# Optimization experiments

Hardware: AMD Instinct MI355X
Metric: run time of the kernel (lower is better)

## Reference

```python
import jax, jax.numpy as jnp
import numpy as np

N_FREQS = 6  # PositionEmbedding default used by LISA


def setup_inputs() -> dict:
    key = jax.random.key(0)
    ks = jax.random.split(key, 8)
    B, L, N, D, H = 8, 32768, 2048, 64, 256
    in_dim = 1 * (2 * N_FREQS + 1) + 3 * D  # 13 + 192 = 205

    def w(k, i, o):
        return jax.random.normal(k, (i, o), jnp.float32) * (1.0 / np.sqrt(i))

    return {
        "coord": jax.random.uniform(ks[0], (B, L, 1), jnp.float32),
        "latent": jax.random.normal(ks[1], (B, N, D), jnp.float32),
        "W0": w(ks[2], in_dim, H), "b0": jnp.zeros((H,), jnp.float32),
        "W1": w(ks[3], H, H), "b1": jnp.zeros((H,), jnp.float32),
        "W2": w(ks[4], H, H), "b2": jnp.zeros((H,), jnp.float32),
        "W3": w(ks[5], H, H), "b3": jnp.zeros((H,), jnp.float32),
        "W4": w(ks[6], H, 1), "b4": jnp.zeros((1,), jnp.float32),
    }


def reference(coord, latent, W0, b0, W1, b1, W2, b2, W3, b3, W4, b4):
    B, N, D = latent.shape
    # feat_unfold: concat shifted-prev / self / shifted-next along channels
    feat = jnp.swapaxes(latent, 1, 2)                                   # [B, D, N]
    feat_prev = jnp.concatenate([feat[:, :, :1], feat[:, :, :-1]], axis=2)
    feat_next = jnp.concatenate([feat[:, :, 1:], feat[:, :, -1:]], axis=2)
    feat = jnp.concatenate([feat_prev, feat, feat_next], axis=1)        # [B, 3D, N]

    # grid_sample(bilinear, padding_mode='border', align_corners=False) on a
    # 1-row image: y coordinate 0 hits row 0 exactly, so only x interpolates.
    # torch mapping: ix = ((gx + 1) * W - 1) / 2 with gx = coord*2 - 1
    ix = coord[..., 0] * N - 0.5                                        # [B, L]
    x0 = jnp.floor(ix)
    t = ix - x0                                                         # lerp weight
    i0 = jnp.clip(x0.astype(jnp.int32), 0, N - 1)                       # border clamp
    i1 = jnp.clip(x0.astype(jnp.int32) + 1, 0, N - 1)
    f0 = jnp.take_along_axis(feat, i0[:, None, :], axis=2)              # [B, 3D, L]
    f1 = jnp.take_along_axis(feat, i1[:, None, :], axis=2)
    sampled = (1.0 - t)[:, None, :] * f0 + t[:, None, :] * f1
    sampled = jnp.swapaxes(sampled, 1, 2)                               # [B, L, 3D]

    # positional encoding: [x, sin(f x), cos(f x) for f in 1,2,4,8,16,32]
    freqs = 2.0 ** jnp.arange(N_FREQS, dtype=jnp.float32)
    ang = coord * freqs                                                 # [B, L, 6]
    pe = jnp.stack([jnp.sin(ang), jnp.cos(ang)], axis=-1)
    pe = pe.reshape(ang.shape[0], ang.shape[1], 2 * N_FREQS)            # [B, L, 12]

    inp = jnp.concatenate([coord, pe, sampled], axis=-1)                # [B, L, 205]

    h = jax.nn.relu(inp @ W0 + b0)
    h = jax.nn.relu(h @ W1 + b1)
    h = jax.nn.relu(h @ W2 + b2)
    h = jax.nn.relu(h @ W3 + b3)
    return h @ W4 + b4                                                  # [B, L, 1]
```

## Files before the change

kernel.cpp:

```cpp
#include <hip/hip_runtime.h>

typedef unsigned short ushort_t;
typedef unsigned int uint_t;
typedef __attribute__((ext_vector_type(8))) short short8;
typedef __attribute__((ext_vector_type(4))) float float4v;
typedef __attribute__((ext_vector_type(4))) uint_t uint4v;

#define NLAT 2048
#define DLAT 64

#define PW_BASE 128
#define PW0_OFF 0
#define PW1_OFF 57344
#define PW2_OFF 122880
#define PW3_OFF 188416
#define H7 28672
#define H8 32768

__device__ __forceinline__ float b2f(ushort_t u) {
  union { uint_t i; float f; } v; v.i = ((uint_t)u) << 16; return v.f;
}
__device__ __forceinline__ ushort_t f2b(float f) {
  uint_t x = __float_as_uint(f);
  uint_t r = (x + 0x7fffu + ((x >> 16) & 1u)) >> 16;
  return (ushort_t)r;
}
__device__ __forceinline__ uint_t pack2(float lo, float hi) {
  return (uint_t)f2b(lo) | ((uint_t)f2b(hi) << 16);
}
__device__ __forceinline__ int imin(int a, int b) { return a < b ? a : b; }
__device__ __forceinline__ int imax(int a, int b) { return a > b ? a : b; }

__device__ __forceinline__ float ldv(const float* p, long i)    { return p[i]; }
__device__ __forceinline__ float ldv(const ushort_t* p, long i) { return b2f(p[i]); }
__device__ __forceinline__ void stv(float* p, long i, float v)    { p[i] = v; }
__device__ __forceinline__ void stv(ushort_t* p, long i, float v) { p[i] = f2b(v); }

__device__ __forceinline__ float4 load4f(const float* p) { return *(const float4*)p; }
__device__ __forceinline__ float4 load4f(const ushort_t* p) {
  uint2 u = *(const uint2*)p;
  float4 r;
  r.x = b2f((ushort_t)(u.x & 0xffffu)); r.y = b2f((ushort_t)(u.x >> 16));
  r.z = b2f((ushort_t)(u.y & 0xffffu)); r.w = b2f((ushort_t)(u.y >> 16));
  return r;
}

__device__ __forceinline__ void async_copy16(const ushort_t* g, ushort_t* l) {
  __builtin_amdgcn_global_load_lds(
      (const __attribute__((address_space(1))) void*)g,
      (__attribute__((address_space(3))) void*)l, 16, 0, 0);
}
__device__ __forceinline__ void stage_half(ushort_t* dst, const ushort_t* src,
                                           int chunks, int tid) {
  for (int k = 0; k < chunks; ++k) {
    int i = tid + (k << 9);
    async_copy16(src + (size_t)i * 8, dst + (size_t)i * 8);
  }
}

__global__ void detect_mode(const ushort_t* __restrict__ lat, int* __restrict__ flag) {
  if (threadIdx.x == 0) *flag = 0;
  __syncthreads();
  int big = 0;
  for (int i = threadIdx.x; i < 1024; i += 64) {
    float v = b2f(lat[i]);
    if (!(fabsf(v) < 1e5f)) big = 1;
  }
  if (__any(big) && threadIdx.x == 0) *flag = 1;
}

template <typename TI>
__global__ void pack_w_t(const TI* __restrict__ W0, const TI* __restrict__ W1,
                         const TI* __restrict__ W2, const TI* __restrict__ W3,
                         ushort_t* __restrict__ pw, const int* __restrict__ flag, int want)
{
  if (*flag != want) return;
  int g = blockIdx.x * blockDim.x + threadIdx.x;
  if (g >= 31 * 1024) return;
  int lane = g & 63, q = lane >> 4;
  int mt   = (g >> 6) & 15;
  int ktg  = g >> 10;
  const TI* W; ushort_t* dst; int kt, KT; bool isw0 = false;
  if (ktg < 7)       { W = W0; dst = pw + PW0_OFF; kt = ktg;      KT = 7; isw0 = true; }
  else if (ktg < 15) { W = W1; dst = pw + PW1_OFF; kt = ktg - 7;  KT = 8; }
  else if (ktg < 23) { W = W2; dst = pw + PW2_OFF; kt = ktg - 15; KT = 8; }
  else               { W = W3; dst = pw + PW3_OFF; kt = ktg - 23; KT = 8; }
  int col = mt * 16 + (lane & 15);
  uint_t words[4];
#pragma unroll
  for (int h = 0; h < 4; ++h) {
    ushort_t vv[2];
#pragma unroll
    for (int e = 0; e < 2; ++e) {
      int j = 2 * h + e;
      int f = 32 * kt + 16 * (j >> 2) + 4 * q + (j & 3);
      int row = f;
      if (isw0) row = (f < 192) ? (13 + f) : (f == 192 ? 0 : (f <= 204 ? f - 192 : -1));
      vv[e] = (row >= 0) ? f2b(ldv(W, (long)row * 256 + col)) : (ushort_t)0;
    }
    words[h] = (uint_t)vv[0] | ((uint_t)vv[1] << 16);
  }
  uint4 o; o.x = words[0]; o.y = words[1]; o.z = words[2]; o.w = words[3];
  *(uint4*)(dst + ((size_t)(mt * KT + kt) * 64 + lane) * 8) = o;
}

template <int KT, int MTBASE>
__device__ __forceinline__ void compute_half(float4v (&acc)[16][2],
                                             const uint4v (&hu)[8][2],
                                             const ushort_t* buf, int lane)
{
#pragma unroll
  for (int m = 0; m < 8; ++m) {
    acc[MTBASE + m][0] = (float4v){0.f, 0.f, 0.f, 0.f};
    acc[MTBASE + m][1] = (float4v){0.f, 0.f, 0.f, 0.f};
  }
#pragma unroll
  for (int kt = 0; kt < KT; ++kt) {
    short8 b0 = __builtin_bit_cast(short8, hu[kt][0]);
    short8 b1 = __builtin_bit_cast(short8, hu[kt][1]);
#pragma unroll
    for (int m = 0; m < 8; ++m) {
      short8 a = *(const short8*)&buf[((size_t)(m * KT + kt) * 64 + lane) * 8];
      acc[MTBASE + m][0] = __builtin_amdgcn_mfma_f32_16x16x32_bf16(a, b0, acc[MTBASE + m][0], 0, 0, 0);
      acc[MTBASE + m][1] = __builtin_amdgcn_mfma_f32_16x16x32_bf16(a, b1, acc[MTBASE + m][1], 0, 0, 0);
    }
  }
}

__device__ __forceinline__ void convert_layer(float4v (&acc)[16][2], uint4v (&hu)[8][2],
                                              const float* bwl, int q)
{
#pragma unroll
  for (int mt = 0; mt < 16; ++mt) {
    float4 b4 = *(const float4*)&bwl[mt * 16 + 4 * q];
#pragma unroll
    for (int g = 0; g < 2; ++g) {
      float v0 = fmaxf(acc[mt][g][0] + b4.x, 0.f);
      float v1 = fmaxf(acc[mt][g][1] + b4.y, 0.f);
      float v2 = fmaxf(acc[mt][g][2] + b4.z, 0.f);
      float v3 = fmaxf(acc[mt][g][3] + b4.w, 0.f);
      hu[mt >> 1][g][(mt & 1) * 2 + 0] = pack2(v0, v1);
      hu[mt >> 1][g][(mt & 1) * 2 + 1] = pack2(v2, v3);
    }
  }
}

template <typename TI>
__global__ __launch_bounds__(512, 2) void lisa_fused_t(
    const TI* __restrict__ coord, const TI* __restrict__ latent,
    const TI* __restrict__ bias0, const TI* __restrict__ bias1,
    const TI* __restrict__ bias2, const TI* __restrict__ bias3,
    const TI* __restrict__ W4,    const TI* __restrict__ b4,
    const ushort_t* __restrict__ pw, TI* __restrict__ out,
    const int* __restrict__ flag, int want)
{
  if (*flag != want) return;
  __shared__ __align__(16) ushort_t wbuf[2][H8];
  __shared__ __align__(16) float bw[4 * 256 + 256 + 1];

  const int tid  = threadIdx.x;
  const int lane = tid & 63, q = lane >> 4, m15 = lane & 15;
  const int wv   = tid >> 6;
  const long pbase = (long)blockIdx.x * 256 + wv * 32 + m15;

  stage_half(wbuf[0], pw + PW0_OFF, 7, tid);
  for (int i = tid; i < 1281; i += 512) {
    float v;
    if (i < 256)       v = ldv(bias0, i);
    else if (i < 512)  v = ldv(bias1, i - 256);
    else if (i < 768)  v = ldv(bias2, i - 512);
    else if (i < 1024) v = ldv(bias3, i - 768);
    else if (i < 1280) v = ldv(W4, i - 1024);
    else               v = ldv(b4, 0);
    bw[i] = v;
  }

  uint4v hu[8][2];
#pragma unroll
  for (int g = 0; g < 2; ++g) {
    long p = pbase + g * 16;
    float c   = ldv(coord, p);
    float ixv = c * 2048.0f - 0.5f;
    float x0f = floorf(ixv);
    float t   = ixv - x0f;
    int   x0  = (int)x0f;
    int   i0  = imin(imax(x0, 0), NLAT - 1);
    int   i1  = imin(imax(x0 + 1, 0), NLAT - 1);
    float w0 = 1.0f - t, w1 = t;
    int rows0[3] = { imax(i0 - 1, 0), i0, imin(i0 + 1, NLAT - 1) };
    int rows1[3] = { imax(i1 - 1, 0), i1, imin(i1 + 1, NLAT - 1) };
    const TI* lat = latent + (size_t)(p >> 15) * (NLAT * DLAT);
#pragma unroll
    for (int tb = 0; tb < 12; ++tb) {
      int region = tb >> 2;
      int d0 = 16 * (tb & 3) + 4 * q;
      float4 a = load4f(lat + (long)rows0[region] * DLAT + d0);
      float4 b = load4f(lat + (long)rows1[region] * DLAT + d0);
      hu[tb >> 1][g][(tb & 1) * 2 + 0] = pack2(w0 * a.x + w1 * b.x, w0 * a.y + w1 * b.y);
      hu[tb >> 1][g][(tb & 1) * 2 + 1] = pack2(w0 * a.z + w1 * b.z, w0 * a.w + w1 * b.w);
    }
    float pv[4];
#pragma unroll
    for (int s = 0; s < 4; ++s) {
      int f = 192 + 4 * q + s;
      float v = 0.0f;
      if (f == 192) v = c;
      else if (f <= 204) {
        int i = f - 193;
        float fr = (float)(1 << (i >> 1));
        float ang = c * fr;
        v = (i & 1) ? __cosf(ang) : __sinf(ang);
      }
      pv[s] = v;
    }
    hu[6][g][0] = pack2(pv[0], pv[1]);
    hu[6][g][1] = pack2(pv[2], pv[3]);
    hu[6][g][2] = 0; hu[6][g][3] = 0;
  }
  __syncthreads();

  float4v acc[16][2];

  stage_half(wbuf[1], pw + PW0_OFF + H7, 7, tid);
  compute_half<7, 0>(acc, hu, wbuf[0], lane);
  __syncthreads();
  stage_half(wbuf[0], pw + PW1_OFF, 8, tid);
  compute_half<7, 8>(acc, hu, wbuf[1], lane);
  convert_layer(acc, hu, bw + 0 * 256, q);
  __syncthreads();

  stage_half(wbuf[1], pw + PW1_OFF + H8, 8, tid);
  compute_half<8, 0>(acc, hu, wbuf[0], lane);
  __syncthreads();
  stage_half(wbuf[0], pw + PW2_OFF, 8, tid);
  compute_half<8, 8>(acc, hu, wbuf[1], lane);
  convert_layer(acc, hu, bw + 1 * 256, q);
  __syncthreads();

  stage_half(wbuf[1], pw + PW2_OFF + H8, 8, tid);
  compute_half<8, 0>(acc, hu, wbuf[0], lane);
  __syncthreads();
  stage_half(wbuf[0], pw + PW3_OFF, 8, tid);
  compute_half<8, 8>(acc, hu, wbuf[1], lane);
  convert_layer(acc, hu, bw + 2 * 256, q);
  __syncthreads();

  stage_half(wbuf[1], pw + PW3_OFF + H8, 8, tid);
  compute_half<8, 0>(acc, hu, wbuf[0], lane);
  __syncthreads();
  compute_half<8, 8>(acc, hu, wbuf[1], lane);

  float partial0 = 0.f, partial1 = 0.f;
#pragma unroll
  for (int mt = 0; mt < 16; ++mt) {
    float4 b3v = *(const float4*)&bw[3 * 256 + mt * 16 + 4 * q];
    float4 w4v = *(const float4*)&bw[1024 + mt * 16 + 4 * q];
    float v;
    v = fmaxf(acc[mt][0][0] + b3v.x, 0.f); partial0 += v * w4v.x;
    v = fmaxf(acc[mt][0][1] + b3v.y, 0.f); partial0 += v * w4v.y;
    v = fmaxf(acc[mt][0][2] + b3v.z, 0.f); partial0 += v * w4v.z;
    v = fmaxf(acc[mt][0][3] + b3v.w, 0.f); partial0 += v * w4v.w;
    v = fmaxf(acc[mt][1][0] + b3v.x, 0.f); partial1 += v * w4v.x;
    v = fmaxf(acc[mt][1][1] + b3v.y, 0.f); partial1 += v * w4v.y;
    v = fmaxf(acc[mt][1][2] + b3v.z, 0.f); partial1 += v * w4v.z;
    v = fmaxf(acc[mt][1][3] + b3v.w, 0.f); partial1 += v * w4v.w;
  }
  partial0 += __shfl_xor(partial0, 16, 64);
  partial0 += __shfl_xor(partial0, 32, 64);
  partial1 += __shfl_xor(partial1, 16, 64);
  partial1 += __shfl_xor(partial1, 32, 64);
  if (lane < 16) {
    float bb = bw[1280];
    stv(out, pbase,      partial0 + bb);
    stv(out, pbase + 16, partial1 + bb);
  }
}

extern "C" void kernel_launch(void* const* d_in, const int* in_sizes, int n_in,
                              void* d_out, int out_size, void* d_ws, size_t ws_size,
                              hipStream_t stream) {
  int* flag = (int*)d_ws;
  ushort_t* pw = (ushort_t*)d_ws + PW_BASE;

  detect_mode<<<1, 64, 0, stream>>>((const ushort_t*)d_in[1], flag);

  pack_w_t<float><<<62, 512, 0, stream>>>(
      (const float*)d_in[2], (const float*)d_in[4], (const float*)d_in[6],
      (const float*)d_in[8], pw, flag, 1);
  lisa_fused_t<float><<<1024, 512, 0, stream>>>(
      (const float*)d_in[0], (const float*)d_in[1],
      (const float*)d_in[3], (const float*)d_in[5], (const float*)d_in[7],
      (const float*)d_in[9], (const float*)d_in[10], (const float*)d_in[11],
      pw, (float*)d_out, flag, 1);

  pack_w_t<ushort_t><<<62, 512, 0, stream>>>(
      (const ushort_t*)d_in[2], (const ushort_t*)d_in[4], (const ushort_t*)d_in[6],
      (const ushort_t*)d_in[8], pw, flag, 0);
  lisa_fused_t<ushort_t><<<1024, 512, 0, stream>>>(
      (const ushort_t*)d_in[0], (const ushort_t*)d_in[1],
      (const ushort_t*)d_in[3], (const ushort_t*)d_in[5], (const ushort_t*)d_in[7],
      (const ushort_t*)d_in[9], (const ushort_t*)d_in[10], (const ushort_t*)d_in[11],
      pw, (ushort_t*)d_out, flag, 0);
}
```

Measured before the change: 258.6 us.

## Stream weights in 32-column chunks with ping-pong activations and smaller blocks

Each layer is now processed in 8 output chunks of 32 features. A small double-buffered LDS tile (2x16KB) is refilled per chunk, and activations ping-pong between two register arrays instead of a 16x2 accumulator array. Blocks shrink from 512 to 256 threads with launch bounds of 3 blocks/CU and twice as many blocks, aiming for lower LDS and register use and higher occupancy. In exchange there are many more __syncthreads barriers (one per chunk), and each barrier has less MFMA work to hide weight-load latency.

```diff
diff --git a/kernel.cpp b/kernel.cpp
--- a/kernel.cpp
+++ b/kernel.cpp
@@ -14,8 +14,6 @@
 #define PW1_OFF 57344
 #define PW2_OFF 122880
 #define PW3_OFF 188416
-#define H7 28672
-#define H8 32768
 
 __device__ __forceinline__ float b2f(ushort_t u) {
   union { uint_t i; float f; } v; v.i = ((uint_t)u) << 16; return v.f;
@@ -50,11 +48,19 @@
       (const __attribute__((address_space(1))) void*)g,
       (__attribute__((address_space(3))) void*)l, 16, 0, 0);
 }
-__device__ __forceinline__ void stage_half(ushort_t* dst, const ushort_t* src,
-                                           int chunks, int tid) {
-  for (int k = 0; k < chunks; ++k) {
-    int i = tid + (k << 9);
-    async_copy16(src + (size_t)i * 8, dst + (size_t)i * 8);
+
+__device__ __forceinline__ void stage_idx(int gi, ushort_t* dst,
+                                          const ushort_t* __restrict__ pw, int tid) {
+  int layer = gi >> 3, c = gi & 7;
+  int KT = (gi < 8) ? 7 : 8;
+  int loff = (layer == 0) ? PW0_OFF : (layer == 1) ? PW1_OFF
+           : (layer == 2) ? PW2_OFF : PW3_OFF;
+  const ushort_t* src = pw + loff + c * KT * 1024;
+  int n = KT * 128;
+#pragma unroll
+  for (int r = 0; r < 4; ++r) {
+    int i = tid + (r << 8);
+    if (i < n) async_copy16(src + (size_t)i * 8, dst + (size_t)i * 8);
   }
 }
 
@@ -104,49 +110,75 @@
   *(uint4*)(dst + ((size_t)(mt * KT + kt) * 64 + lane) * 8) = o;
 }
 
-template <int KT, int MTBASE>
-__device__ __forceinline__ void compute_half(float4v (&acc)[16][2],
-                                             const uint4v (&hu)[8][2],
-                                             const ushort_t* buf, int lane)
+template <int KT, int BASE, bool LAST>
+__device__ __forceinline__ void layer_run(
+    uint4v (&hin)[8][2], uint4v (&hout)[8][2],
+    const float* bwl, const float* w4t,
+    ushort_t (*wbuf)[8192], const ushort_t* __restrict__ pw,
+    int tid, int lane, int q,
+    float& partial0, float& partial1)
 {
 #pragma unroll
-  for (int m = 0; m < 8; ++m) {
-    acc[MTBASE + m][0] = (float4v){0.f, 0.f, 0.f, 0.f};
-    acc[MTBASE + m][1] = (float4v){0.f, 0.f, 0.f, 0.f};
-  }
-#pragma unroll
-  for (int kt = 0; kt < KT; ++kt) {
-    short8 b0 = __builtin_bit_cast(short8, hu[kt][0]);
-    short8 b1 = __builtin_bit_cast(short8, hu[kt][1]);
-#pragma unroll
-    for (int m = 0; m < 8; ++m) {
-      short8 a = *(const short8*)&buf[((size_t)(m * KT + kt) * 64 + lane) * 8];
-      acc[MTBASE + m][0] = __builtin_amdgcn_mfma_f32_16x16x32_bf16(a, b0, acc[MTBASE + m][0], 0, 0, 0);
-      acc[MTBASE + m][1] = __builtin_amdgcn_mfma_f32_16x16x32_bf16(a, b1, acc[MTBASE + m][1], 0, 0, 0);
-    }
-  }
-}
-
-__device__ __forceinline__ void convert_layer(float4v (&acc)[16][2], uint4v (&hu)[8][2],
-                                              const float* bwl, int q)
-{
-#pragma unroll
-  for (int mt = 0; mt < 16; ++mt) {
-    float4 b4 = *(const float4*)&bwl[mt * 16 + 4 * q];
-#pragma unroll
-    for (int g = 0; g < 2; ++g) {
-      float v0 = fmaxf(acc[mt][g][0] + b4.x, 0.f);
-      float v1 = fmaxf(acc[mt][g][1] + b4.y, 0.f);
-      float v2 = fmaxf(acc[mt][g][2] + b4.z, 0.f);
-      float v3 = fmaxf(acc[mt][g][3] + b4.w, 0.f);
-      hu[mt >> 1][g][(mt & 1) * 2 + 0] = pack2(v0, v1);
-      hu[mt >> 1][g][(mt & 1) * 2 + 1] = pack2(v2, v3);
-    }
+  for (int c = 0; c < 8; ++c) {
+    constexpr int NB = 8;
+    const int gi = BASE + c;
+    if (gi + 1 < 32) stage_idx(gi + 1, wbuf[(gi + 1) & 1], pw, tid);
+    const ushort_t* buf = wbuf[gi & 1];
+
+    float4v acc[2][2];
+#pragma unroll
+    for (int m = 0; m < 2; ++m) {
+      acc[m][0] = (float4v){0.f, 0.f, 0.f, 0.f};
+      acc[m][1] = (float4v){0.f, 0.f, 0.f, 0.f};
+    }
+#pragma unroll
+    for (int kt = 0; kt < KT; ++kt) {
+      short8 b0 = __builtin_bit_cast(short8, hin[kt][0]);
+      short8 b1 = __builtin_bit_cast(short8, hin[kt][1]);
+#pragma unroll
+      for (int m = 0; m < 2; ++m) {
+        short8 a = *(const short8*)&buf[((size_t)(m * KT + kt) * 64 + lane) * 8];
+        acc[m][0] = __builtin_amdgcn_mfma_f32_16x16x32_bf16(a, b0, acc[m][0], 0, 0, 0);
+        acc[m][1] = __builtin_amdgcn_mfma_f32_16x16x32_bf16(a, b1, acc[m][1], 0, 0, 0);
+      }
+    }
+    if constexpr (!LAST) {
+#pragma unroll
+      for (int m = 0; m < 2; ++m) {
+        float4 bv = *(const float4*)&bwl[(2 * c + m) * 16 + 4 * q];
+#pragma unroll
+        for (int g = 0; g < 2; ++g) {
+          float v0 = fmaxf(acc[m][g][0] + bv.x, 0.f);
+          float v1 = fmaxf(acc[m][g][1] + bv.y, 0.f);
+          float v2 = fmaxf(acc[m][g][2] + bv.z, 0.f);
+          float v3 = fmaxf(acc[m][g][3] + bv.w, 0.f);
+          hout[c][g][m * 2 + 0] = pack2(v0, v1);
+          hout[c][g][m * 2 + 1] = pack2(v2, v3);
+        }
+      }
+    } else {
+#pragma unroll
+      for (int m = 0; m < 2; ++m) {
+        float4 bv  = *(const float4*)&bwl[(2 * c + m) * 16 + 4 * q];
+        float4 wv4 = *(const float4*)&w4t[(2 * c + m) * 16 + 4 * q];
+        float v;
+        v = fmaxf(acc[m][0][0] + bv.x, 0.f); partial0 += v * wv4.x;
+        v = fmaxf(acc[m][0][1] + bv.y, 0.f); partial0 += v * wv4.y;
+        v = fmaxf(acc[m][0][2] + bv.z, 0.f); partial0 += v * wv4.z;
+        v = fmaxf(acc[m][0][3] + bv.w, 0.f); partial0 += v * wv4.w;
+        v = fmaxf(acc[m][1][0] + bv.x, 0.f); partial1 += v * wv4.x;
+        v = fmaxf(acc[m][1][1] + bv.y, 0.f); partial1 += v * wv4.y;
+        v = fmaxf(acc[m][1][2] + bv.z, 0.f); partial1 += v * wv4.z;
+        v = fmaxf(acc[m][1][3] + bv.w, 0.f); partial1 += v * wv4.w;
+      }
+    }
+    __syncthreads();
+    (void)NB;
   }
 }
 
 template <typename TI>
-__global__ __launch_bounds__(512, 2) void lisa_fused_t(
+__global__ __launch_bounds__(256, 3) void lisa_fused_t(
     const TI* __restrict__ coord, const TI* __restrict__ latent,
     const TI* __restrict__ bias0, const TI* __restrict__ bias1,
     const TI* __restrict__ bias2, const TI* __restrict__ bias3,
@@ -155,16 +187,16 @@
     const int* __restrict__ flag, int want)
 {
   if (*flag != want) return;
-  __shared__ __align__(16) ushort_t wbuf[2][H8];
+  __shared__ __align__(16) ushort_t wbuf[2][8192];
   __shared__ __align__(16) float bw[4 * 256 + 256 + 1];
 
   const int tid  = threadIdx.x;
   const int lane = tid & 63, q = lane >> 4, m15 = lane & 15;
   const int wv   = tid >> 6;
-  const long pbase = (long)blockIdx.x * 256 + wv * 32 + m15;
-
-  stage_half(wbuf[0], pw + PW0_OFF, 7, tid);
-  for (int i = tid; i < 1281; i += 512) {
+  const long pbase = (long)blockIdx.x * 128 + wv * 32 + m15;
+
+  stage_idx(0, wbuf[0], pw, tid);
+  for (int i = tid; i < 1281; i += 256) {
     float v;
     if (i < 256)       v = ldv(bias0, i);
     else if (i < 512)  v = ldv(bias1, i - 256);
@@ -175,7 +207,7 @@
     bw[i] = v;
   }
 
-  uint4v hu[8][2];
+  uint4v huA[8][2], huB[8][2];
 #pragma unroll
   for (int g = 0; g < 2; ++g) {
     long p = pbase + g * 16;
@@ -196,8 +228,8 @@
       int d0 = 16 * (tb & 3) + 4 * q;
       float4 a = load4f(lat + (long)rows0[region] * DLAT + d0);
       float4 b = load4f(lat + (long)rows1[region] * DLAT + d0);
-      hu[tb >> 1][g][(tb & 1) * 2 + 0] = pack2(w0 * a.x + w1 * b.x, w0 * a.y + w1 * b.y);
-      hu[tb >> 1][g][(tb & 1) * 2 + 1] = pack2(w0 * a.z + w1 * b.z, w0 * a.w + w1 * b.w);
+      huA[tb >> 1][g][(tb & 1) * 2 + 0] = pack2(w0 * a.x + w1 * b.x, w0 * a.y + w1 * b.y);
+      huA[tb >> 1][g][(tb & 1) * 2 + 1] = pack2(w0 * a.z + w1 * b.z, w0 * a.w + w1 * b.w);
     }
     float pv[4];
 #pragma unroll
@@ -213,58 +245,18 @@
       }
       pv[s] = v;
     }
-    hu[6][g][0] = pack2(pv[0], pv[1]);
-    hu[6][g][1] = pack2(pv[2], pv[3]);
-    hu[6][g][2] = 0; hu[6][g][3] = 0;
+    huA[6][g][0] = pack2(pv[0], pv[1]);
+    huA[6][g][1] = pack2(pv[2], pv[3]);
+    huA[6][g][2] = 0; huA[6][g][3] = 0;
   }
   __syncthreads();
 
-  float4v acc[16][2];
-
-  stage_half(wbuf[1], pw + PW0_OFF + H7, 7, tid);
-  compute_half<7, 0>(acc, hu, wbuf[0], lane);
-  __syncthreads();
-  stage_half(wbuf[0], pw + PW1_OFF, 8, tid);
-  compute_half<7, 8>(acc, hu, wbuf[1], lane);
-  convert_layer(acc, hu, bw + 0 * 256, q);
-  __syncthreads();
-
-  stage_half(wbuf[1], pw + PW1_OFF + H8, 8, tid);
-  compute_half<8, 0>(acc, hu, wbuf[0], lane);
-  __syncthreads();
-  stage_half(wbuf[0], pw + PW2_OFF, 8, tid);
-  compute_half<8, 8>(acc, hu, wbuf[1], lane);
-  convert_layer(acc, hu, bw + 1 * 256, q);
-  __syncthreads();
-
-  stage_half(wbuf[1], pw + PW2_OFF + H8, 8, tid);
-  compute_half<8, 0>(acc, hu, wbuf[0], lane);
-  __syncthreads();
-  stage_half(wbuf[0], pw + PW3_OFF, 8, tid);
-  compute_half<8, 8>(acc, hu, wbuf[1], lane);
-  convert_layer(acc, hu, bw + 2 * 256, q);
-  __syncthreads();
-
-  stage_half(wbuf[1], pw + PW3_OFF + H8, 8, tid);
-  compute_half<8, 0>(acc, hu, wbuf[0], lane);
-  __syncthreads();
-  compute_half<8, 8>(acc, hu, wbuf[1], lane);
-
   float partial0 = 0.f, partial1 = 0.f;
-#pragma unroll
-  for (int mt = 0; mt < 16; ++mt) {
-    float4 b3v = *(const float4*)&bw[3 * 256 + mt * 16 + 4 * q];
-    float4 w4v = *(const float4*)&bw[1024 + mt * 16 + 4 * q];
-    float v;
-    v = fmaxf(acc[mt][0][0] + b3v.x, 0.f); partial0 += v * w4v.x;
-    v = fmaxf(acc[mt][0][1] + b3v.y, 0.f); partial0 += v * w4v.y;
-    v = fmaxf(acc[mt][0][2] + b3v.z, 0.f); partial0 += v * w4v.z;
-    v = fmaxf(acc[mt][0][3] + b3v.w, 0.f); partial0 += v * w4v.w;
-    v = fmaxf(acc[mt][1][0] + b3v.x, 0.f); partial1 += v * w4v.x;
-    v = fmaxf(acc[mt][1][1] + b3v.y, 0.f); partial1 += v * w4v.y;
-    v = fmaxf(acc[mt][1][2] + b3v.z, 0.f); partial1 += v * w4v.z;
-    v = fmaxf(acc[mt][1][3] + b3v.w, 0.f); partial1 += v * w4v.w;
-  }
+  layer_run<7,  0, false>(huA, huB, bw + 0 * 256, bw + 1024, wbuf, pw, tid, lane, q, partial0, partial1);
+  layer_run<8,  8, false>(huB, huA, bw + 1 * 256, bw + 1024, wbuf, pw, tid, lane, q, partial0, partial1);
+  layer_run<8, 16, false>(huA, huB, bw + 2 * 256, bw + 1024, wbuf, pw, tid, lane, q, partial0, partial1);
+  layer_run<8, 24, true >(huB, huA, bw + 3 * 256, bw + 1024, wbuf, pw, tid, lane, q, partial0, partial1);
+
   partial0 += __shfl_xor(partial0, 16, 64);
   partial0 += __shfl_xor(partial0, 32, 64);
   partial1 += __shfl_xor(partial1, 16, 64);
@@ -287,7 +279,7 @@
   pack_w_t<float><<<62, 512, 0, stream>>>(
       (const float*)d_in[2], (const float*)d_in[4], (const float*)d_in[6],
       (const float*)d_in[8], pw, flag, 1);
-  lisa_fused_t<float><<<1024, 512, 0, stream>>>(
+  lisa_fused_t<float><<<2048, 256, 0, stream>>>(
       (const float*)d_in[0], (const float*)d_in[1],
       (const float*)d_in[3], (const float*)d_in[5], (const float*)d_in[7],
       (const float*)d_in[9], (const float*)d_in[10], (const float*)d_in[11],
@@ -296,7 +288,7 @@
   pack_w_t<ushort_t><<<62, 512, 0, stream>>>(
       (const ushort_t*)d_in[2], (const ushort_t*)d_in[4], (const ushort_t*)d_in[6],
       (const ushort_t*)d_in[8], pw, flag, 0);
-  lisa_fused_t<ushort_t><<<1024, 512, 0, stream>>>(
+  lisa_fused_t<ushort_t><<<2048, 256, 0, stream>>>(
       (const ushort_t*)d_in[0], (const ushort_t*)d_in[1],
       (const ushort_t*)d_in[3], (const ushort_t*)d_in[5], (const ushort_t*)d_in[7],
       (const ushort_t*)d_in[9], (const ushort_t*)d_in[10], (const ushort_t*)d_in[11],
```

New measurement: 448.7 us. 1.74x slower.

## Shrink blocks to 256 threads and stream weights in quarter-layer double buffers

Applied to the files above, without the earlier changes.

The fused MLP kernel moves from 512-thread blocks with half-layer weight buffers (2x64KB LDS) to 256-thread blocks with quarter-layer buffers (2x32KB). The grid doubles so each block handles 128 points. Each layer is now split into four stages with prefetch of the next quarter and a barrier after each. This cuts LDS per block so more blocks can be resident per CU and overlap loads with MFMA. The cost is twice as many weight loads from L2 per point and more barriers. The bf16 pack also switches from the manual rounding routine to the HIP intrinsic conversion.

```diff
diff --git a/kernel.cpp b/kernel.cpp
--- a/kernel.cpp
+++ b/kernel.cpp
@@ -1,4 +1,5 @@
 #include <hip/hip_runtime.h>
+#include <hip/hip_bf16.h>
 
 typedef unsigned short ushort_t;
 typedef unsigned int uint_t;
@@ -14,8 +15,6 @@
 #define PW1_OFF 57344
 #define PW2_OFF 122880
 #define PW3_OFF 188416
-#define H7 28672
-#define H8 32768
 
 __device__ __forceinline__ float b2f(ushort_t u) {
   union { uint_t i; float f; } v; v.i = ((uint_t)u) << 16; return v.f;
@@ -26,7 +25,10 @@
   return (ushort_t)r;
 }
 __device__ __forceinline__ uint_t pack2(float lo, float hi) {
-  return (uint_t)f2b(lo) | ((uint_t)f2b(hi) << 16);
+  float2 t; t.x = lo; t.y = hi;
+  union { __hip_bfloat162 h; uint_t u; } cv;
+  cv.h = __float22bfloat162_rn(t);
+  return cv.u;
 }
 __device__ __forceinline__ int imin(int a, int b) { return a < b ? a : b; }
 __device__ __forceinline__ int imax(int a, int b) { return a > b ? a : b; }
@@ -50,12 +52,17 @@
       (const __attribute__((address_space(1))) void*)g,
       (__attribute__((address_space(3))) void*)l, 16, 0, 0);
 }
-__device__ __forceinline__ void stage_half(ushort_t* dst, const ushort_t* src,
-                                           int chunks, int tid) {
-  for (int k = 0; k < chunks; ++k) {
-    int i = tid + (k << 9);
+
+__device__ __forceinline__ void stage_q(int gi, ushort_t* dst,
+                                        const ushort_t* __restrict__ pw, int tid) {
+  int layer = gi >> 2, q = gi & 3;
+  int KT = (layer == 0) ? 7 : 8;
+  int loff = (layer == 0) ? PW0_OFF : (layer == 1) ? PW1_OFF
+           : (layer == 2) ? PW2_OFF : PW3_OFF;
+  const ushort_t* src = pw + loff + q * KT * 2048;
+  int n = KT * 256;
+  for (int i = tid; i < n; i += 256)
     async_copy16(src + (size_t)i * 8, dst + (size_t)i * 8);
-  }
 }
 
 __global__ void detect_mode(const ushort_t* __restrict__ lat, int* __restrict__ flag) {
@@ -104,26 +111,35 @@
   *(uint4*)(dst + ((size_t)(mt * KT + kt) * 64 + lane) * 8) = o;
 }
 
-template <int KT, int MTBASE>
-__device__ __forceinline__ void compute_half(float4v (&acc)[16][2],
-                                             const uint4v (&hu)[8][2],
-                                             const ushort_t* buf, int lane)
-{
-#pragma unroll
-  for (int m = 0; m < 8; ++m) {
-    acc[MTBASE + m][0] = (float4v){0.f, 0.f, 0.f, 0.f};
-    acc[MTBASE + m][1] = (float4v){0.f, 0.f, 0.f, 0.f};
-  }
-#pragma unroll
-  for (int kt = 0; kt < KT; ++kt) {
-    short8 b0 = __builtin_bit_cast(short8, hu[kt][0]);
-    short8 b1 = __builtin_bit_cast(short8, hu[kt][1]);
-#pragma unroll
-    for (int m = 0; m < 8; ++m) {
-      short8 a = *(const short8*)&buf[((size_t)(m * KT + kt) * 64 + lane) * 8];
-      acc[MTBASE + m][0] = __builtin_amdgcn_mfma_f32_16x16x32_bf16(a, b0, acc[MTBASE + m][0], 0, 0, 0);
-      acc[MTBASE + m][1] = __builtin_amdgcn_mfma_f32_16x16x32_bf16(a, b1, acc[MTBASE + m][1], 0, 0, 0);
-    }
+template <int KT>
+__device__ __forceinline__ void run_layer(int base, float4v (&acc)[16][2],
+                                          const uint4v (&hu)[8][2],
+                                          ushort_t (*wbuf)[16384],
+                                          const ushort_t* __restrict__ pw,
+                                          int tid, int lane)
+{
+#pragma unroll
+  for (int qq = 0; qq < 4; ++qq) {
+    const int gi = base + qq;
+    if (gi + 1 < 16) stage_q(gi + 1, wbuf[(gi + 1) & 1], pw, tid);
+    const ushort_t* buf = wbuf[gi & 1];
+#pragma unroll
+    for (int m = 0; m < 4; ++m) {
+      acc[qq * 4 + m][0] = (float4v){0.f, 0.f, 0.f, 0.f};
+      acc[qq * 4 + m][1] = (float4v){0.f, 0.f, 0.f, 0.f};
+    }
+#pragma unroll
+    for (int kt = 0; kt < KT; ++kt) {
+      short8 b0 = __builtin_bit_cast(short8, hu[kt][0]);
+      short8 b1 = __builtin_bit_cast(short8, hu[kt][1]);
+#pragma unroll
+      for (int m = 0; m < 4; ++m) {
+        short8 a = *(const short8*)&buf[((size_t)(m * KT + kt) * 64 + lane) * 8];
+        acc[qq * 4 + m][0] = __builtin_amdgcn_mfma_f32_16x16x32_bf16(a, b0, acc[qq * 4 + m][0], 0, 0, 0);
+        acc[qq * 4 + m][1] = __builtin_amdgcn_mfma_f32_16x16x32_bf16(a, b1, acc[qq * 4 + m][1], 0, 0, 0);
+      }
+    }
+    __syncthreads();
   }
 }
 
@@ -146,7 +162,7 @@
 }
 
 template <typename TI>
-__global__ __launch_bounds__(512, 2) void lisa_fused_t(
+__global__ __launch_bounds__(256, 2) void lisa_fused_t(
     const TI* __restrict__ coord, const TI* __restrict__ latent,
     const TI* __restrict__ bias0, const TI* __restrict__ bias1,
     const TI* __restrict__ bias2, const TI* __restrict__ bias3,
@@ -155,16 +171,16 @@
     const int* __restrict__ flag, int want)
 {
   if (*flag != want) return;
-  __shared__ __align__(16) ushort_t wbuf[2][H8];
+  __shared__ __align__(16) ushort_t wbuf[2][16384];
   __shared__ __align__(16) float bw[4 * 256 + 256 + 1];
 
   const int tid  = threadIdx.x;
   const int lane = tid & 63, q = lane >> 4, m15 = lane & 15;
   const int wv   = tid >> 6;
-  const long pbase = (long)blockIdx.x * 256 + wv * 32 + m15;
-
-  stage_half(wbuf[0], pw + PW0_OFF, 7, tid);
-  for (int i = tid; i < 1281; i += 512) {
+  const long pbase = (long)blockIdx.x * 128 + wv * 32 + m15;
+
+  stage_q(0, wbuf[0], pw, tid);
+  for (int i = tid; i < 1281; i += 256) {
     float v;
     if (i < 256)       v = ldv(bias0, i);
     else if (i < 512)  v = ldv(bias1, i - 256);
@@ -221,34 +237,13 @@
 
   float4v acc[16][2];
 
-  stage_half(wbuf[1], pw + PW0_OFF + H7, 7, tid);
-  compute_half<7, 0>(acc, hu, wbuf[0], lane);
-  __syncthreads();
-  stage_half(wbuf[0], pw + PW1_OFF, 8, tid);
-  compute_half<7, 8>(acc, hu, wbuf[1], lane);
+  run_layer<7>( 0, acc, hu, wbuf, pw, tid, lane);
   convert_layer(acc, hu, bw + 0 * 256, q);
-  __syncthreads();
-
-  stage_half(wbuf[1], pw + PW1_OFF + H8, 8, tid);
-  compute_half<8, 0>(acc, hu, wbuf[0], lane);
-  __syncthreads();
-  stage_half(wbuf[0], pw + PW2_OFF, 8, tid);
-  compute_half<8, 8>(acc, hu, wbuf[1], lane);
+  run_layer<8>( 4, acc, hu, wbuf, pw, tid, lane);
   convert_layer(acc, hu, bw + 1 * 256, q);
-  __syncthreads();
-
-  stage_half(wbuf[1], pw + PW2_OFF + H8, 8, tid);
-  compute_half<8, 0>(acc, hu, wbuf[0], lane);
-  __syncthreads();
-  stage_half(wbuf[0], pw + PW3_OFF, 8, tid);
-  compute_half<8, 8>(acc, hu, wbuf[1], lane);
+  run_layer<8>( 8, acc, hu, wbuf, pw, tid, lane);
   convert_layer(acc, hu, bw + 2 * 256, q);
-  __syncthreads();
-
-  stage_half(wbuf[1], pw + PW3_OFF + H8, 8, tid);
-  compute_half<8, 0>(acc, hu, wbuf[0], lane);
-  __syncthreads();
-  compute_half<8, 8>(acc, hu, wbuf[1], lane);
+  run_layer<8>(12, acc, hu, wbuf, pw, tid, lane);
 
   float partial0 = 0.f, partial1 = 0.f;
 #pragma unroll
@@ -287,7 +282,7 @@
   pack_w_t<float><<<62, 512, 0, stream>>>(
       (const float*)d_in[2], (const float*)d_in[4], (const float*)d_in[6],
       (const float*)d_in[8], pw, flag, 1);
-  lisa_fused_t<float><<<1024, 512, 0, stream>>>(
+  lisa_fused_t<float><<<2048, 256, 0, stream>>>(
       (const float*)d_in[0], (const float*)d_in[1],
       (const float*)d_in[3], (const float*)d_in[5], (const float*)d_in[7],
       (const float*)d_in[9], (const float*)d_in[10], (const float*)d_in[11],
@@ -296,7 +291,7 @@
   pack_w_t<ushort_t><<<62, 512, 0, stream>>>(
       (const ushort_t*)d_in[2], (const ushort_t*)d_in[4], (const ushort_t*)d_in[6],
       (const ushort_t*)d_in[8], pw, flag, 0);
-  lisa_fused_t<ushort_t><<<1024, 512, 0, stream>>>(
+  lisa_fused_t<ushort_t><<<2048, 256, 0, stream>>>(
       (const ushort_t*)d_in[0], (const ushort_t*)d_in[1],
       (const ushort_t*)d_in[3], (const ushort_t*)d_in[5], (const ushort_t*)d_in[7],
       (const ushort_t*)d_in[9], (const ushort_t*)d_in[10], (const ushort_t*)d_in[11],
```

Measured after the change: 236.7 us. -8.5%, faster.
